# Performance work log

Measured on AMD Instinct MI355X. Metric: run time of the kernel, lower is better.

The kernel has to match this reference:

```python
import jax, jax.numpy as jnp
import numpy as np

B, A, G = 16, 32, 512      # batch, atoms, g_feat_in
S, M = 1024, 8             # subset samples, peaks per subset
E, OH = 5, 20              # element types, thermometer size per element
FE = E * OH                # formula encoding = 100
D = 512                    # internal_d
NBINS = 512                # spect bins
EPS = 1e-4


def _ln(x, g, b):
    m = x.mean(-1, keepdims=True)
    v = jnp.mean((x - m) ** 2, -1, keepdims=True)
    return (x - m) * jax.lax.rsqrt(v + 1e-5) * g + b


def setup_inputs() -> dict:
    key = jax.random.key(0)
    ks = jax.random.split(key, 16)
    vert_feat_in = jax.random.normal(ks[0], (B, A, G), jnp.float32)
    vert_mask_in = jnp.ones((B, A), jnp.float32)
    elem = jax.random.randint(ks[1], (B, A), 0, E)
    vert_element_oh = jax.nn.one_hot(elem, E, dtype=jnp.float32)
    atom_subsets = jax.random.randint(ks[2], (B, S, A), 0, 2).astype(jnp.int32)
    atom_subsets_peaks_mass_idx = jax.random.randint(ks[3], (B, S, M), 0, NBINS).astype(jnp.int32)
    atom_subsets_peaks_intensity = jax.random.uniform(ks[4], (B, S, M), jnp.float32)

    def lin(k, o, i):
        s = 1.0 / np.sqrt(i)
        return jax.random.uniform(k, (o, i), jnp.float32, -s, s)

    return dict(
        vert_feat_in=vert_feat_in, vert_mask_in=vert_mask_in,
        vert_element_oh=vert_element_oh, atom_subsets=atom_subsets,
        atom_subsets_peaks_mass_idx=atom_subsets_peaks_mass_idx,
        atom_subsets_peaks_intensity=atom_subsets_peaks_intensity,
        ln_sub_g=jnp.ones((G,)), ln_sub_b=jnp.zeros((G,)),
        W_ih=lin(ks[5], 3 * G, FE), W_hh=lin(ks[6], 3 * G, G),
        b_ih=jnp.zeros((3 * G,)), b_hh=jnp.zeros((3 * G,)),
        ln_post_g=jnp.ones((G,)), ln_post_b=jnp.zeros((G,)),
        W1=lin(ks[7], D, G), b1=jnp.zeros((D,)),
        W2a=lin(ks[8], D, D), b2a=jnp.zeros((D,)),
        W2b=lin(ks[9], D, D), b2b=jnp.zeros((D,)),
        ln_pre_g=jnp.ones((D,)), ln_pre_b=jnp.zeros((D,)),
        W_s=lin(ks[10], 1, D), b_s=jnp.zeros((1,)),
    )


def reference(vert_feat_in, vert_mask_in, vert_element_oh, atom_subsets,
              atom_subsets_peaks_mass_idx, atom_subsets_peaks_intensity,
              ln_sub_g, ln_sub_b, W_ih, W_hh, b_ih, b_hh,
              ln_post_g, ln_post_b, W1, b1, W2a, b2a, W2b, b2b,
              ln_pre_g, ln_pre_b, W_s, b_s):
    subs_f = atom_subsets.astype(jnp.float32)
    masked_vert = vert_feat_in * vert_mask_in[:, :, None]          # B,A,G
    subs_masked = subs_f * vert_mask_in[:, None, :]                 # B,S,A
    # subset-weighted pooling of vertex features
    swv_sum = jnp.einsum('baf,bsa->bsf', masked_vert, subs_masked)  # B,S,G
    subset_size = subs_masked.sum(-1) + EPS                         # B,S
    swv_mean = swv_sum / subset_size[..., None]
    h = _ln(swv_mean, ln_sub_g, ln_sub_b)                           # B,S,G
    # formula counts -> thermometer (accumulating) one-hot; .byte() cast kills grads
    counts = jax.lax.stop_gradient(
        jnp.einsum('bae,bsa->bse', vert_element_oh, subs_f))        # B,S,E
    therm = (jnp.arange(OH, dtype=jnp.float32)[None, None, None, :] < counts[..., None])
    formulae = therm.astype(jnp.float32).reshape(counts.shape[0], counts.shape[1], FE)
    # GRUCell: input=formula encoding, hidden=subset_normed
    gi = jnp.einsum('bsf,gf->bsg', formulae, W_ih) + b_ih           # B,S,3G
    gh = jnp.einsum('bsh,gh->bsg', h, W_hh) + b_hh
    gi_r, gi_z, gi_n = jnp.split(gi, 3, axis=-1)
    gh_r, gh_z, gh_n = jnp.split(gh, 3, axis=-1)
    r = jax.nn.sigmoid(gi_r + gh_r)
    z = jax.nn.sigmoid(gi_z + gh_z)
    n = jnp.tanh(gi_n + r * gh_n)
    combined = (1.0 - z) * n + z * h                                # B,S,G
    x = _ln(combined, ln_post_g, ln_post_b)
    x = jax.nn.relu(jnp.einsum('bsg,dg->bsd', x, W1) + b1)
    x = jax.nn.relu(jnp.einsum('bsd,ed->bse', x, W2a) + b2a)
    x = jax.nn.relu(jnp.einsum('bsd,ed->bse', x, W2b) + b2b)
    x = _ln(x, ln_pre_g, ln_pre_b)
    scores = (jnp.einsum('bsd,od->bso', x, W_s) + b_s)[..., 0]      # B,S
    probs = jax.nn.softmax(scores, axis=-1)                         # B,S
    # sparse mass-matrix multiply: scatter subset probs into spectrum bins
    weighted = atom_subsets_peaks_intensity * probs[:, :, None]     # B,S,M
    bidx = jnp.arange(probs.shape[0])[:, None, None]
    spect_out = jnp.zeros((probs.shape[0], NBINS), probs.dtype)
    spect_out = spect_out.at[bidx, atom_subsets_peaks_mass_idx].add(weighted)
    return spect_out, probs
```

## Files before the change

### kernel.cpp

```cpp
#include <hip/hip_runtime.h>

#define NB 16
#define NA 32
#define NG 512
#define NS 1024
#define NM 8
#define NE 5
#define NOH 20
#define NFE 100
#define ND 512
#define NBINS 512
#define NTOK (NB * NS)

typedef unsigned short ushort_t;
typedef __attribute__((ext_vector_type(8))) short bf16x8;
typedef __attribute__((ext_vector_type(4))) float f32x4;

__device__ __forceinline__ ushort_t f2bf(float x) {
  union { float f; unsigned u; } v; v.f = x;
  unsigned r = v.u + 0x7FFF + ((v.u >> 16) & 1);
  return (ushort_t)(r >> 16);
}
__device__ __forceinline__ float bf2f(ushort_t b) {
  union { unsigned u; float f; } v; v.u = ((unsigned)b) << 16;
  return v.f;
}

__device__ __forceinline__ void gload_lds16(const void* g, void* l) {
  __builtin_amdgcn_global_load_lds(
      (const __attribute__((address_space(1))) void*)g,
      (__attribute__((address_space(3))) void*)l, 16, 0, 0);
}

__device__ __forceinline__ float wsum64(float v) {
#pragma unroll
  for (int off = 32; off > 0; off >>= 1) v += __shfl_xor(v, off);
  return v;
}

__global__ __launch_bounds__(256) void setup_kernel(
    const float* __restrict__ vert, const float* __restrict__ mask,
    const float* __restrict__ eloh, const int* __restrict__ subs,
    const float* __restrict__ Wih, const float* __restrict__ Whh,
    const float* __restrict__ W1, const float* __restrict__ W2a,
    const float* __restrict__ W2b,
    float* __restrict__ tcd, float* __restrict__ PS,
    ushort_t* __restrict__ o_hh, ushort_t* __restrict__ o1,
    ushort_t* __restrict__ o2a, ushort_t* __restrict__ o2b,
    ushort_t* __restrict__ VmT, ushort_t* __restrict__ S_bf) {
  int i = blockIdx.x * 256 + threadIdx.x;
  if (i < NTOK) {
    int b = i >> 10;
    const int* srow = subs + (size_t)i * NA;
    float cnt[NE] = {0.f, 0.f, 0.f, 0.f, 0.f};
    float z = 0.f;
    for (int a = 0; a < NA; a++) {
      float sb = (float)srow[a];
      z += sb * mask[b * NA + a];
      const float* eo = eloh + (size_t)(b * NA + a) * NE;
#pragma unroll
      for (int e = 0; e < NE; e++) cnt[e] += eo[e] * sb;
    }
    float* o = tcd + (size_t)i * 8;
#pragma unroll
    for (int e = 0; e < NE; e++) o[e] = cnt[e];
    o[5] = 1.0f / (z + 1e-4f);
    return;
  }
  i -= NTOK;
  if (i < NE * 1536) {
    int e = i / 1536, g = i % 1536;
    float s = 0.f;
    float* base = PS + ((size_t)e * 21) * 1536 + g;
    base[0] = 0.f;
    for (int c = 1; c <= NOH; c++) {
      s += Wih[(size_t)g * NFE + e * NOH + (c - 1)];
      base[(size_t)c * 1536] = s;
    }
    return;
  }
  i -= NE * 1536;
  if (i < 1536 * NG) { o_hh[i] = f2bf(Whh[i]); return; }
  i -= 1536 * NG;
  if (i < ND * NG) { o1[i] = f2bf(W1[i]); return; }
  i -= ND * NG;
  if (i < ND * ND) { o2a[i] = f2bf(W2a[i]); return; }
  i -= ND * ND;
  if (i < ND * ND) { o2b[i] = f2bf(W2b[i]); return; }
  i -= ND * ND;
  const int nV = NB * NG * NA;
  if (i < nV) {
    int b = i / (NG * NA); int rem = i % (NG * NA);
    int f = rem >> 5, a = rem & 31;
    float mk = mask[b * NA + a];
    VmT[i] = f2bf(vert[(size_t)b * NA * NG + a * NG + f] * mk * mk);
    return;
  }
  i -= nV;
  if (i < NTOK * NA) S_bf[i] = f2bf((float)subs[i]);
}

__global__ __launch_bounds__(256) void pool_gemm(
    const ushort_t* __restrict__ S_bf, const ushort_t* __restrict__ VmT,
    const float* __restrict__ tcd, float* __restrict__ SWV, int tok0) {
  __shared__ ushort_t As[128 * 32];
  __shared__ ushort_t Bs[128 * 32];
  const int t = threadIdx.x;
  const int w = t >> 6, lane = t & 63;
  const int wr = w >> 1, wc = w & 1;
  const int bm = blockIdx.x * 128;
  const int bn = blockIdx.y * 128;
  const int b = (tok0 + bm) >> 10;
  const int srow = lane >> 2;
  const int scol = (((lane & 3) ^ ((lane >> 3) & 3)) * 8);
  const ushort_t* Bbase = VmT + (size_t)b * NG * NA;
  gload_lds16(S_bf + (size_t)(tok0 + bm + w * 16 + srow) * 32 + scol, &As[w * 512]);
  gload_lds16(S_bf + (size_t)(tok0 + bm + 64 + w * 16 + srow) * 32 + scol, &As[2048 + w * 512]);
  gload_lds16(Bbase + (size_t)(bn + w * 16 + srow) * 32 + scol, &Bs[w * 512]);
  gload_lds16(Bbase + (size_t)(bn + 64 + w * 16 + srow) * 32 + scol, &Bs[2048 + w * 512]);
  __syncthreads();

  const int lr = lane & 15, lq = lane >> 4;
  const int rchunk = (lq ^ ((lr >> 1) & 3)) * 8;
  f32x4 acc[4][4];
#pragma unroll
  for (int m = 0; m < 4; m++)
#pragma unroll
    for (int n = 0; n < 4; n++) acc[m][n] = (f32x4)0.f;
  bf16x8 a[4], bb[4];
#pragma unroll
  for (int m = 0; m < 4; m++)
    a[m] = *(const bf16x8*)&As[(wr * 64 + m * 16 + lr) * 32 + rchunk];
#pragma unroll
  for (int n = 0; n < 4; n++)
    bb[n] = *(const bf16x8*)&Bs[(wc * 64 + n * 16 + lr) * 32 + rchunk];
#pragma unroll
  for (int m = 0; m < 4; m++)
#pragma unroll
    for (int n = 0; n < 4; n++)
      acc[m][n] = __builtin_amdgcn_mfma_f32_16x16x32_bf16(a[m], bb[n], acc[m][n], 0, 0, 0);

#pragma unroll
  for (int n = 0; n < 4; n++) {
    const int col = bn + wc * 64 + n * 16 + lr;
#pragma unroll
    for (int m = 0; m < 4; m++) {
      f32x4 v = acc[m][n];
#pragma unroll
      for (int r = 0; r < 4; r++) {
        int row = bm + wr * 64 + m * 16 + lq * 4 + r;
        float inv = tcd[(size_t)(tok0 + row) * 8 + 5];
        SWV[(size_t)row * NG + col] = v[r] * inv;
      }
    }
  }
}

__global__ __launch_bounds__(256) void finish_kernel(
    const float* __restrict__ SWV, const float* __restrict__ lng,
    const float* __restrict__ lnb, ushort_t* __restrict__ Hb) {
  const int t = threadIdx.x;
  const int lane = t & 63, wv = t >> 6;
  const int ltok = blockIdx.x * 4 + wv;
  const int f = lane * 8;
  const float* row = SWV + (size_t)ltok * NG + f;
  float4 v0 = *(const float4*)row;
  float4 v1 = *(const float4*)(row + 4);
  float x[8] = {v0.x, v0.y, v0.z, v0.w, v1.x, v1.y, v1.z, v1.w};
  float ps = 0.f;
#pragma unroll
  for (int j = 0; j < 8; j++) ps += x[j];
  float mean = wsum64(ps) * (1.0f / NG);
  float pq = 0.f;
#pragma unroll
  for (int j = 0; j < 8; j++) { float d = x[j] - mean; pq += d * d; }
  float rstd = rsqrtf(wsum64(pq) * (1.0f / NG) + 1e-5f);
  float4 g0 = *(const float4*)&lng[f], g1 = *(const float4*)&lng[f + 4];
  float4 b0 = *(const float4*)&lnb[f], b1 = *(const float4*)&lnb[f + 4];
  float gg[8] = {g0.x, g0.y, g0.z, g0.w, g1.x, g1.y, g1.z, g1.w};
  float bbv[8] = {b0.x, b0.y, b0.z, b0.w, b1.x, b1.y, b1.z, b1.w};
  bf16x8 ho;
#pragma unroll
  for (int j = 0; j < 8; j++) ho[j] = (short)f2bf((x[j] - mean) * rstd * gg[j] + bbv[j]);
  *(bf16x8*)&Hb[(size_t)ltok * NG + f] = ho;
}

__global__ __launch_bounds__(256) void gemm_bf16(
    const ushort_t* __restrict__ A, const ushort_t* __restrict__ W,
    const float* __restrict__ bias, ushort_t* __restrict__ C,
    int K, int Dout, int mode) {
  __shared__ ushort_t As[2][4096];
  __shared__ ushort_t Bs[2][4096];
  const int t = threadIdx.x;
  const int w = t >> 6;
  const int lane = t & 63;
  const int wr = w >> 1, wc = w & 1;
  const int bm = blockIdx.x * 128, bn = blockIdx.y * 128;

  const int srow = lane >> 2;
  const int scol = (((lane & 3) ^ ((lane >> 3) & 3)) * 8);
  const ushort_t* Ag0 = A + (size_t)(bm + w * 16 + srow) * K + scol;
  const ushort_t* Ag1 = A + (size_t)(bm + 64 + w * 16 + srow) * K + scol;
  const ushort_t* Wg0 = W + (size_t)(bn + w * 16 + srow) * K + scol;
  const ushort_t* Wg1 = W + (size_t)(bn + 64 + w * 16 + srow) * K + scol;
  const int l0 = w * 512;
  const int l1 = 2048 + w * 512;

  const int lr = lane & 15;
  const int lq = lane >> 4;
  const int rchunk = (lq ^ ((lr >> 1) & 3)) * 8;

  f32x4 acc[4][4];
#pragma unroll
  for (int m = 0; m < 4; m++)
#pragma unroll
    for (int n = 0; n < 4; n++) acc[m][n] = (f32x4)0.f;

  gload_lds16(Ag0, &As[0][l0]);
  gload_lds16(Ag1, &As[0][l1]);
  gload_lds16(Wg0, &Bs[0][l0]);
  gload_lds16(Wg1, &Bs[0][l1]);
  __syncthreads();

  const int nk = K >> 5;
  int cur = 0;
  for (int kt = 0; kt < nk; kt++) {
    if (kt + 1 < nk) {
      const int k1 = (kt + 1) << 5;
      gload_lds16(Ag0 + k1, &As[cur ^ 1][l0]);
      gload_lds16(Ag1 + k1, &As[cur ^ 1][l1]);
      gload_lds16(Wg0 + k1, &Bs[cur ^ 1][l0]);
      gload_lds16(Wg1 + k1, &Bs[cur ^ 1][l1]);
    }
    bf16x8 a[4], b[4];
#pragma unroll
    for (int m = 0; m < 4; m++)
      a[m] = *(const bf16x8*)&As[cur][(wr * 64 + m * 16 + lr) * 32 + rchunk];
#pragma unroll
    for (int n = 0; n < 4; n++)
      b[n] = *(const bf16x8*)&Bs[cur][(wc * 64 + n * 16 + lr) * 32 + rchunk];
#pragma unroll
    for (int m = 0; m < 4; m++)
#pragma unroll
      for (int n = 0; n < 4; n++)
        acc[m][n] = __builtin_amdgcn_mfma_f32_16x16x32_bf16(a[m], b[n], acc[m][n], 0, 0, 0);
    __syncthreads();
    cur ^= 1;
  }

#pragma unroll
  for (int n = 0; n < 4; n++) {
    const int col = bn + wc * 64 + n * 16 + lr;
    const float bv = bias[col];
#pragma unroll
    for (int m = 0; m < 4; m++) {
      f32x4 v = acc[m][n];
#pragma unroll
      for (int r = 0; r < 4; r++) {
        int row = bm + wr * 64 + m * 16 + lq * 4 + r;
        float u = v[r] + bv;
        if (mode == 1) u = fmaxf(u, 0.f);
        C[(size_t)row * Dout + col] = f2bf(u);
      }
    }
  }
}

__global__ __launch_bounds__(256) void gate_ln_kernel(
    const ushort_t* __restrict__ Gh, const ushort_t* __restrict__ Hb,
    const float* __restrict__ tcd, const float* __restrict__ PS,
    const float* __restrict__ b_ih, const float* __restrict__ lng,
    const float* __restrict__ lnb, ushort_t* __restrict__ X0) {
  const int t = threadIdx.x;
  const int lane = t & 63, wv = t >> 6;
  const int ltok = blockIdx.x * 4 + wv;
  const int f = lane * 8;
  int c[NE];
#pragma unroll
  for (int e = 0; e < NE; e++) {
    int ci = (int)tcd[(size_t)ltok * 8 + e];
    c[e] = ci > NOH ? NOH : ci;
  }
  float4 r0 = *(const float4*)&b_ih[f],          r1 = *(const float4*)&b_ih[f + 4];
  float4 z0 = *(const float4*)&b_ih[NG + f],     z1 = *(const float4*)&b_ih[NG + f + 4];
  float4 n0 = *(const float4*)&b_ih[2 * NG + f], n1 = *(const float4*)&b_ih[2 * NG + f + 4];
#pragma unroll
  for (int e = 0; e < NE; e++) {
    const float* pe = PS + ((size_t)(e * 21 + c[e])) * 1536;
    r0 += *(const float4*)&pe[f];          r1 += *(const float4*)&pe[f + 4];
    z0 += *(const float4*)&pe[NG + f];     z1 += *(const float4*)&pe[NG + f + 4];
    n0 += *(const float4*)&pe[2 * NG + f]; n1 += *(const float4*)&pe[2 * NG + f + 4];
  }
  float gir[8] = {r0.x, r0.y, r0.z, r0.w, r1.x, r1.y, r1.z, r1.w};
  float giz[8] = {z0.x, z0.y, z0.z, z0.w, z1.x, z1.y, z1.z, z1.w};
  float gin[8] = {n0.x, n0.y, n0.z, n0.w, n1.x, n1.y, n1.z, n1.w};

  const ushort_t* gh = Gh + (size_t)ltok * 1536;
  bf16x8 vr = *(const bf16x8*)&gh[f];
  bf16x8 vz = *(const bf16x8*)&gh[NG + f];
  bf16x8 vn = *(const bf16x8*)&gh[2 * NG + f];
  bf16x8 vh = *(const bf16x8*)&Hb[(size_t)ltok * NG + f];
  float cv[8];
  float ps = 0.f;
#pragma unroll
  for (int j = 0; j < 8; j++) {
    float rg = 1.f / (1.f + expf(-(gir[j] + bf2f((ushort_t)vr[j]))));
    float zg = 1.f / (1.f + expf(-(giz[j] + bf2f((ushort_t)vz[j]))));
    float ng = tanhf(gin[j] + rg * bf2f((ushort_t)vn[j]));
    cv[j] = (1.f - zg) * ng + zg * bf2f((ushort_t)vh[j]);
    ps += cv[j];
  }
  float mean = wsum64(ps) * (1.0f / NG);
  float pq = 0.f;
#pragma unroll
  for (int j = 0; j < 8; j++) { float d = cv[j] - mean; pq += d * d; }
  float rstd = rsqrtf(wsum64(pq) * (1.0f / NG) + 1e-5f);
  float4 g0 = *(const float4*)&lng[f], g1 = *(const float4*)&lng[f + 4];
  float4 b0 = *(const float4*)&lnb[f], b1 = *(const float4*)&lnb[f + 4];
  float gg[8] = {g0.x, g0.y, g0.z, g0.w, g1.x, g1.y, g1.z, g1.w};
  float bbv[8] = {b0.x, b0.y, b0.z, b0.w, b1.x, b1.y, b1.z, b1.w};
  bf16x8 xo;
#pragma unroll
  for (int j = 0; j < 8; j++) xo[j] = (short)f2bf((cv[j] - mean) * rstd * gg[j] + bbv[j]);
  *(bf16x8*)&X0[(size_t)ltok * NG + f] = xo;
}

__global__ __launch_bounds__(256) void ln_score_kernel(
    const ushort_t* __restrict__ X, const float* __restrict__ lng,
    const float* __restrict__ lnb, const float* __restrict__ Wsc,
    const float* __restrict__ bsc, float* __restrict__ scores) {
  const int t = threadIdx.x;
  const int lane = t & 63, wv = t >> 6;
  const int ltok = blockIdx.x * 4 + wv;
  const int f = lane * 8;
  bf16x8 xx = *(const bf16x8*)&X[(size_t)ltok * ND + f];
  float x[8];
  float ps = 0.f;
#pragma unroll
  for (int j = 0; j < 8; j++) { x[j] = bf2f((ushort_t)xx[j]); ps += x[j]; }
  float mean = wsum64(ps) * (1.0f / ND);
  float pq = 0.f;
#pragma unroll
  for (int j = 0; j < 8; j++) { float d = x[j] - mean; pq += d * d; }
  float rstd = rsqrtf(wsum64(pq) * (1.0f / ND) + 1e-5f);
  float4 g0 = *(const float4*)&lng[f], g1 = *(const float4*)&lng[f + 4];
  float4 b0 = *(const float4*)&lnb[f], b1 = *(const float4*)&lnb[f + 4];
  float4 w0 = *(const float4*)&Wsc[f], w1 = *(const float4*)&Wsc[f + 4];
  float gg[8] = {g0.x, g0.y, g0.z, g0.w, g1.x, g1.y, g1.z, g1.w};
  float bbv[8] = {b0.x, b0.y, b0.z, b0.w, b1.x, b1.y, b1.z, b1.w};
  float ww[8] = {w0.x, w0.y, w0.z, w0.w, w1.x, w1.y, w1.z, w1.w};
  float d = 0.f;
#pragma unroll
  for (int j = 0; j < 8; j++) d += ((x[j] - mean) * rstd * gg[j] + bbv[j]) * ww[j];
  float dot = wsum64(d);
  if (lane == 0) scores[ltok] = dot + bsc[0];
}

__global__ __launch_bounds__(256) void softmax_scatter_kernel(
    const float* __restrict__ scores, const int* __restrict__ pidx,
    const float* __restrict__ pint, float* __restrict__ spect,
    float* __restrict__ probs) {
  const int b = blockIdx.x;
  const int t = threadIdx.x;
  __shared__ float s_red[4];
  __shared__ float s_spec[NBINS];
  const float* sc = scores + (size_t)b * NS;
  float v[4];
  float mx = -1e30f;
#pragma unroll
  for (int i = 0; i < 4; i++) { v[i] = sc[t + i * 256]; mx = fmaxf(mx, v[i]); }
#pragma unroll
  for (int off = 32; off > 0; off >>= 1) mx = fmaxf(mx, __shfl_down(mx, off));
  if ((t & 63) == 0) s_red[t >> 6] = mx;
  __syncthreads();
  mx = fmaxf(fmaxf(s_red[0], s_red[1]), fmaxf(s_red[2], s_red[3]));
  float e[4], sum = 0.f;
#pragma unroll
  for (int i = 0; i < 4; i++) { e[i] = expf(v[i] - mx); sum += e[i]; }
#pragma unroll
  for (int off = 32; off > 0; off >>= 1) sum += __shfl_down(sum, off);
  __syncthreads();
  if ((t & 63) == 0) s_red[t >> 6] = sum;
  __syncthreads();
  sum = s_red[0] + s_red[1] + s_red[2] + s_red[3];
  float inv = 1.f / sum;
  s_spec[t] = 0.f; s_spec[t + 256] = 0.f;
  float p[4];
#pragma unroll
  for (int i = 0; i < 4; i++) {
    p[i] = e[i] * inv;
    probs[(size_t)b * NS + t + i * 256] = p[i];
  }
  __syncthreads();
#pragma unroll
  for (int i = 0; i < 4; i++) {
    const int s = t + i * 256;
    const int* idx = pidx + ((size_t)b * NS + s) * NM;
    const float* wt = pint + ((size_t)b * NS + s) * NM;
#pragma unroll
    for (int m = 0; m < NM; m++)
      atomicAdd(&s_spec[idx[m]], wt[m] * p[i]);
  }
  __syncthreads();
  spect[(size_t)b * NBINS + t] = s_spec[t];
  spect[(size_t)b * NBINS + t + 256] = s_spec[t + 256];
}

extern "C" void kernel_launch(void* const* d_in, const int* in_sizes, int n_in,
                              void* d_out, int out_size, void* d_ws, size_t ws_size,
                              hipStream_t stream) {
  const float* vert = (const float*)d_in[0];
  const float* mask = (const float*)d_in[1];
  const float* eloh = (const float*)d_in[2];
  const int* subs = (const int*)d_in[3];
  const int* pidx = (const int*)d_in[4];
  const float* pint = (const float*)d_in[5];
  const float* ln_sub_g = (const float*)d_in[6];
  const float* ln_sub_b = (const float*)d_in[7];
  const float* W_ih = (const float*)d_in[8];
  const float* W_hh = (const float*)d_in[9];
  const float* b_ih = (const float*)d_in[10];
  const float* b_hh = (const float*)d_in[11];
  const float* ln_post_g = (const float*)d_in[12];
  const float* ln_post_b = (const float*)d_in[13];
  const float* W1 = (const float*)d_in[14];
  const float* b1 = (const float*)d_in[15];
  const float* W2a = (const float*)d_in[16];
  const float* b2a = (const float*)d_in[17];
  const float* W2b = (const float*)d_in[18];
  const float* b2b = (const float*)d_in[19];
  const float* ln_pre_g = (const float*)d_in[20];
  const float* ln_pre_b = (const float*)d_in[21];
  const float* W_s = (const float*)d_in[22];
  const float* b_s = (const float*)d_in[23];

  float* out = (float*)d_out;
  float* probs = out + NB * NBINS;

  char* ws = (char*)d_ws;
  float* scores = (float*)ws;
  ushort_t* Whh_bf = (ushort_t*)(ws + 65536);
  ushort_t* W1_bf  = (ushort_t*)(ws + 1638400);
  ushort_t* W2a_bf = (ushort_t*)(ws + 2162688);
  ushort_t* W2b_bf = (ushort_t*)(ws + 2686976);
  ushort_t* VmT    = (ushort_t*)(ws + 3211264);
  ushort_t* S_bf   = (ushort_t*)(ws + 3735552);
  float*    tcd    = (float*)(ws + 4784128);
  float*    PS     = (float*)(ws + 5308416);
  const size_t fixed = 5953536;

  const size_t per_tok = 7168;
  int T = NTOK;
  while (T > 1024 && fixed + (size_t)T * per_tok > ws_size) T >>= 1;
  const int nchunks = NTOK / T;

  char* cb = ws + fixed;
  float*    SWV = (float*)cb;                             cb += (size_t)T * 2048;
  ushort_t* Hb  = (ushort_t*)cb;                          cb += (size_t)T * 1024;
  ushort_t* Gh  = (ushort_t*)cb;                          cb += (size_t)T * 3072;
  ushort_t* X0  = (ushort_t*)cb;
  ushort_t* X1  = Gh;
  ushort_t* X2  = Gh + (size_t)T * 512;
  ushort_t* X3  = X0;

  const int setup_items = NTOK + NE * 1536 + 1536 * NG + ND * NG + 2 * ND * ND
                        + NB * NG * NA + NTOK * NA;
  setup_kernel<<<(setup_items + 255) / 256, 256, 0, stream>>>(
      vert, mask, eloh, subs, W_ih, W_hh, W1, W2a, W2b,
      tcd, PS, Whh_bf, W1_bf, W2a_bf, W2b_bf, VmT, S_bf);

  for (int c = 0; c < nchunks; c++) {
    const int tok0 = c * T;

    dim3 gp(T / 128, NG / 128);
    pool_gemm<<<gp, 256, 0, stream>>>(S_bf, VmT, tcd, SWV, tok0);
    finish_kernel<<<T / 4, 256, 0, stream>>>(SWV, ln_sub_g, ln_sub_b, Hb);

    dim3 g1(T / 128, 1536 / 128);
    gemm_bf16<<<g1, 256, 0, stream>>>(Hb, Whh_bf, b_hh, Gh, NG, 1536, 3);

    gate_ln_kernel<<<T / 4, 256, 0, stream>>>(Gh, Hb, tcd + (size_t)tok0 * 8, PS,
                                              b_ih, ln_post_g, ln_post_b, X0);

    dim3 g2(T / 128, ND / 128);
    gemm_bf16<<<g2, 256, 0, stream>>>(X0, W1_bf, b1, X1, NG, ND, 1);
    gemm_bf16<<<g2, 256, 0, stream>>>(X1, W2a_bf, b2a, X2, ND, ND, 1);
    gemm_bf16<<<g2, 256, 0, stream>>>(X2, W2b_bf, b2b, X3, ND, ND, 1);

    ln_score_kernel<<<T / 4, 256, 0, stream>>>(X3, ln_pre_g, ln_pre_b, W_s, b_s,
                                               scores + tok0);
  }

  softmax_scatter_kernel<<<NB, 256, 0, stream>>>(scores, pidx, pint, out, probs);
}
```

Baseline: 270.2 us.

## Triple-buffer GEMM LDS staging with partial vmcnt waits and MFMA priority

Measured after the change: 269.3 us. No clear change (-0.4%).

```diff
diff --git a/kernel.cpp b/kernel.cpp
--- a/kernel.cpp
+++ b/kernel.cpp
@@ -189,8 +189,8 @@
     const ushort_t* __restrict__ A, const ushort_t* __restrict__ W,
     const float* __restrict__ bias, ushort_t* __restrict__ C,
     int K, int Dout, int mode) {
-  __shared__ ushort_t As[2][4096];
-  __shared__ ushort_t Bs[2][4096];
+  __shared__ ushort_t As[3][4096];
+  __shared__ ushort_t Bs[3][4096];
   const int t = threadIdx.x;
   const int w = t >> 6;
   const int lane = t & 63;
@@ -216,37 +216,57 @@
 #pragma unroll
     for (int n = 0; n < 4; n++) acc[m][n] = (f32x4)0.f;
 
-  gload_lds16(Ag0, &As[0][l0]);
-  gload_lds16(Ag1, &As[0][l1]);
-  gload_lds16(Wg0, &Bs[0][l0]);
-  gload_lds16(Wg1, &Bs[0][l1]);
-  __syncthreads();
-
   const int nk = K >> 5;
-  int cur = 0;
+
+#define STAGE(buf, kt)                                   \
+  do {                                                   \
+    const int kk_ = (kt) << 5;                           \
+    gload_lds16(Ag0 + kk_, &As[(buf)][l0]);              \
+    gload_lds16(Ag1 + kk_, &As[(buf)][l1]);              \
+    gload_lds16(Wg0 + kk_, &Bs[(buf)][l0]);              \
+    gload_lds16(Wg1 + kk_, &Bs[(buf)][l1]);              \
+  } while (0)
+
+  STAGE(0, 0);
+  if (nk > 1) {
+    STAGE(1, 1);
+    asm volatile("s_waitcnt vmcnt(4)" ::: "memory");
+  } else {
+    asm volatile("s_waitcnt vmcnt(0)" ::: "memory");
+  }
+  __builtin_amdgcn_sched_barrier(0);
+  __builtin_amdgcn_s_barrier();
+  __builtin_amdgcn_sched_barrier(0);
+
+  int c0 = 0;
   for (int kt = 0; kt < nk; kt++) {
-    if (kt + 1 < nk) {
-      const int k1 = (kt + 1) << 5;
-      gload_lds16(Ag0 + k1, &As[cur ^ 1][l0]);
-      gload_lds16(Ag1 + k1, &As[cur ^ 1][l1]);
-      gload_lds16(Wg0 + k1, &Bs[cur ^ 1][l0]);
-      gload_lds16(Wg1 + k1, &Bs[cur ^ 1][l1]);
-    }
+    const int c2 = (c0 >= 1) ? c0 - 1 : c0 + 2;
+    if (kt + 2 < nk) STAGE(c2, kt + 2);
     bf16x8 a[4], b[4];
 #pragma unroll
     for (int m = 0; m < 4; m++)
-      a[m] = *(const bf16x8*)&As[cur][(wr * 64 + m * 16 + lr) * 32 + rchunk];
+      a[m] = *(const bf16x8*)&As[c0][(wr * 64 + m * 16 + lr) * 32 + rchunk];
 #pragma unroll
     for (int n = 0; n < 4; n++)
-      b[n] = *(const bf16x8*)&Bs[cur][(wc * 64 + n * 16 + lr) * 32 + rchunk];
+      b[n] = *(const bf16x8*)&Bs[c0][(wc * 64 + n * 16 + lr) * 32 + rchunk];
+    __builtin_amdgcn_s_setprio(1);
 #pragma unroll
     for (int m = 0; m < 4; m++)
 #pragma unroll
       for (int n = 0; n < 4; n++)
         acc[m][n] = __builtin_amdgcn_mfma_f32_16x16x32_bf16(a[m], b[n], acc[m][n], 0, 0, 0);
-    __syncthreads();
-    cur ^= 1;
-  }
+    __builtin_amdgcn_s_setprio(0);
+    if (kt + 2 < nk) {
+      asm volatile("s_waitcnt vmcnt(4)" ::: "memory");
+    } else if (kt + 1 < nk) {
+      asm volatile("s_waitcnt vmcnt(0)" ::: "memory");
+    }
+    __builtin_amdgcn_sched_barrier(0);
+    __builtin_amdgcn_s_barrier();
+    __builtin_amdgcn_sched_barrier(0);
+    c0 = (c0 >= 2) ? 0 : c0 + 1;
+  }
+#undef STAGE
 
 #pragma unroll
   for (int n = 0; n < 4; n++) {
```
